# Optimization experiments

Hardware: AMD Instinct MI355X
Metric: run time of the kernel (lower is better)

## Reference

```python
import jax, jax.numpy as jnp
from jax import lax
import numpy as np

B, S, D, COMP = 4, 1024, 512, 4


def setup_inputs() -> dict:
    key = jax.random.key(0)
    x = jax.random.normal(key, (B * S, D), dtype=jnp.float32)
    return {"x": x, "comp_rate": COMP, "seqlen": S}


def _merge_step(x, t, seq):
    # x: [seq, D], compacted so the k = seq - t valid tokens occupy rows 0..k-1.
    xn = jnp.roll(x, -1, axis=0)  # x[i+1] (wrap value never selected among valid pairs)
    # dist only feeds argmax (non-differentiable), mirror torch exactly; stop_gradient
    # keeps the vjp from saving residuals for this dead-for-gradients path.
    xg = lax.stop_gradient(x)
    dist = jnp.sum(xg * jnp.roll(xg, -1, axis=0), axis=-1)  # scalar_product metric
    j = jnp.arange(x.shape[0])
    dist = jnp.where(j < seq - 1 - t, dist, -jnp.inf)  # k-1 valid adjacent pairs
    mid = jnp.argmax(dist)
    jm = j[:, None]
    # rows < mid keep, row mid becomes (x[mid]+x[mid+1])/2, rows > mid shift left by 1
    return jnp.where(jm < mid, x, jnp.where(jm == mid, (x + xn) * 0.5, xn))


def _merge_sample(x, steps, seq):
    def body(carry, t):
        return _merge_step(carry, t, seq), None
    x, _ = lax.scan(body, x, jnp.arange(steps))
    return x


def reference(x, comp_rate, seqlen):
    d = x.shape[-1]
    b = x.shape[0] // seqlen
    n_comp = seqlen // comp_rate
    steps = seqlen - n_comp
    xb = x.reshape(b, seqlen, d)
    merged = jax.vmap(lambda xs: _merge_sample(xs, steps, seqlen))(xb)
    # torch smart_merge concatenates per-sample results along dim 0
    return merged[:, :n_comp].reshape(b * n_comp, d)
```

## Files before the change

kernel.cpp:

```cpp
#include <hip/hip_runtime.h>
#include <math.h>

#define S 1024
#define D 512
#define NCOMP (S / 4)
#define STEPS (S - NCOMP)
#define NEG_INF (-__builtin_inff())

__device__ __forceinline__ int   f2i(float x) { return __builtin_bit_cast(int, x); }
__device__ __forceinline__ float i2f(int x)   { return __builtin_bit_cast(float, x); }

__device__ __forceinline__ unsigned fkey(float f) {
    unsigned u = __builtin_bit_cast(unsigned, f);
    return (u & 0x80000000u) ? ~u : (u | 0x80000000u);
}
__device__ __forceinline__ float unfkey(unsigned k) {
    unsigned u = (k & 0x80000000u) ? (k & 0x7fffffffu) : ~k;
    return __builtin_bit_cast(float, u);
}

__device__ __forceinline__ float wave_sum63(float x) {
    x += i2f(__builtin_amdgcn_update_dpp(0, f2i(x), 0x111, 0xF, 0xF, true));
    x += i2f(__builtin_amdgcn_update_dpp(0, f2i(x), 0x112, 0xF, 0xF, true));
    x += i2f(__builtin_amdgcn_update_dpp(0, f2i(x), 0x114, 0xF, 0xF, true));
    x += i2f(__builtin_amdgcn_update_dpp(0, f2i(x), 0x118, 0xF, 0xF, true));
    x += i2f(__builtin_amdgcn_update_dpp(0, f2i(x), 0x142, 0xA, 0xF, true));
    x += i2f(__builtin_amdgcn_update_dpp(0, f2i(x), 0x143, 0xC, 0xF, true));
    return x;
}

#define AMAX_STEP(ctrl, rm) do {                                                        \
    unsigned ok_ = (unsigned)__builtin_amdgcn_update_dpp((int)key, (int)key, (ctrl), (rm), 0xF, false); \
    int      oi_ = __builtin_amdgcn_update_dpp(bi, bi, (ctrl), (rm), 0xF, false);        \
    bool tk_ = (ok_ > key) || ((ok_ == key) && (oi_ < bi));                              \
    key = tk_ ? ok_ : key; bi = tk_ ? oi_ : bi;                                          \
} while (0)

struct Row { float4 a, b; };

__device__ __forceinline__ Row row_load(const float* vals, int slot, int lane) {
    const float4* p = (const float4*)(vals + (size_t)slot * D);
    Row r; r.a = p[lane * 2]; r.b = p[lane * 2 + 1]; return r;
}
__device__ __forceinline__ void row_store(float* vals, int slot, int lane, Row r) {
    float4* p = (float4*)(vals + (size_t)slot * D);
    p[lane * 2] = r.a; p[lane * 2 + 1] = r.b;
}
__device__ __forceinline__ Row row_avg(Row x, Row y) {
    Row r;
    r.a.x = (x.a.x + y.a.x) * 0.5f; r.a.y = (x.a.y + y.a.y) * 0.5f;
    r.a.z = (x.a.z + y.a.z) * 0.5f; r.a.w = (x.a.w + y.a.w) * 0.5f;
    r.b.x = (x.b.x + y.b.x) * 0.5f; r.b.y = (x.b.y + y.b.y) * 0.5f;
    r.b.z = (x.b.z + y.b.z) * 0.5f; r.b.w = (x.b.w + y.b.w) * 0.5f;
    return r;
}
__device__ __forceinline__ float dot8_partial(Row x, Row y) {
    float acc = x.a.x * y.a.x;
    acc += x.a.y * y.a.y; acc += x.a.z * y.a.z; acc += x.a.w * y.a.w;
    acc += x.b.x * y.b.x; acc += x.b.y * y.b.y; acc += x.b.z * y.b.z; acc += x.b.w * y.b.w;
    return acc;
}
__device__ __forceinline__ int lsr(int s) { return ((unsigned)s < (unsigned)S) ? s : 0; }
__device__ __forceinline__ int lsl(int s) { return ((unsigned)s <= (unsigned)S) ? s : 0; }

__device__ __forceinline__ void lds_argmax(const float* dist, int lane, float& v1, int& i1) {
    float av[16];
#pragma unroll
    for (int k = 0; k < 16; ++k) av[k] = dist[lane + 64 * k];
    float v8[8]; int k8[8];
#pragma unroll
    for (int k = 0; k < 8; ++k) { bool tk = av[k+8] > av[k]; v8[k] = tk ? av[k+8] : av[k]; k8[k] = tk ? (k+8) : k; }
    float v4[4]; int k4[4];
#pragma unroll
    for (int k = 0; k < 4; ++k) { bool tk = v8[k+4] > v8[k]; v4[k] = tk ? v8[k+4] : v8[k]; k4[k] = tk ? k8[k+4] : k8[k]; }
    float v2[2]; int k2[2];
#pragma unroll
    for (int k = 0; k < 2; ++k) { bool tk = v4[k+2] > v4[k]; v2[k] = tk ? v4[k+2] : v4[k]; k2[k] = tk ? k4[k+2] : k4[k]; }
    bool tk1 = v2[1] > v2[0];
    float lv = tk1 ? v2[1] : v2[0];
    int   lk = tk1 ? k2[1] : k2[0];
    unsigned key = fkey(lv);
    int bi = lane | (lk << 6);
    AMAX_STEP(0x111, 0xF); AMAX_STEP(0x112, 0xF);
    AMAX_STEP(0x114, 0xF); AMAX_STEP(0x118, 0xF);
    AMAX_STEP(0x142, 0xA); AMAX_STEP(0x143, 0xC);
    i1 = __builtin_amdgcn_readlane(bi, 63);
    v1 = unfkey((unsigned)__builtin_amdgcn_readlane((int)key, 63));
}

__global__ __launch_bounds__(256) void init_kernel(const float* __restrict__ x,
                                                   float* __restrict__ vals,
                                                   float* __restrict__ out) {
    const int blk = blockIdx.x, b = blk >> 4, g = blk & 15;
    const int tid = threadIdx.x, lane = tid & 63, w = tid >> 6;
    const float* xb = x + (size_t)b * S * D;
    if (vals != x) {
        float* vb = vals + (size_t)b * S * D;
        const float4* s4 = (const float4*)xb;
        float4* d4 = (float4*)vb;
        const int base = g * (S * D / 4 / 16);
        for (int i = tid; i < S * D / 4 / 16; i += 256) d4[base + i] = s4[base + i];
    }
    float* sd = out + (size_t)b * NCOMP * D;
#pragma unroll 1
    for (int j = 0; j < 16; ++j) {
        int pr = g * 64 + w * 16 + j;
        if (pr < S - 1) {
            Row A = row_load(xb, pr, lane);
            Row B = row_load(xb, pr + 1, lane);
            float t = wave_sum63(dot8_partial(A, B));
            if (lane == 63) sd[pr] = t;
        }
    }
    if (g == 0 && tid == 0) sd[S - 1] = NEG_INF;
}

__global__ __launch_bounds__(64) void merge_kernel(float* __restrict__ vals,
                                                   float* __restrict__ out) {
    const int b = blockIdx.x, lane = threadIdx.x;
    float* vb = vals + (size_t)b * S * D;
    float* aux = out + (size_t)b * NCOMP * D;
    const float* sd = aux;
    int* outIdx = (int*)(aux + S);

    __shared__ int4  links[S + 1];
    __shared__ float dist[S];

#pragma unroll
    for (int k = 0; k < 16; ++k) {
        int s = lane + 64 * k;
        links[s] = make_int4(s - 1, s + 1, (s + 2 <= S) ? (s + 2) : S, 0);
        dist[s] = sd[s];
    }
    if (lane == 0) links[S] = make_int4(S, S, S, 0);

    float v1; int i1;
    lds_argmax(dist, lane, v1, i1);
    int m = i1;
    int4 L0 = links[m];
    int p = __builtin_amdgcn_readfirstlane(L0.x);
    int r = __builtin_amdgcn_readfirstlane(L0.y);
    int q = __builtin_amdgcn_readfirstlane(L0.z);
    bool hasp = (p >= 0), hasq = (q < S);
    int pp = hasp ? __builtin_amdgcn_readfirstlane(links[p].x) : -1;
    int nq = hasq ? __builtin_amdgcn_readfirstlane(links[q].y) : S;
    Row Rp  = row_load(vb, lsr(p),  lane);
    Row Rm  = row_load(vb, m,       lane);
    Row Rr  = row_load(vb, r,       lane);
    Row Rq  = row_load(vb, lsr(q),  lane);
    Row Rpp = row_load(vb, lsr(pp), lane);
    Row Rnq = row_load(vb, lsr(nq), lane);

#pragma unroll 1
    for (int t = 0; t < STEPS; ++t) {
        if (lane == 0) {
            links[m].y = q; links[m].z = nq;
            if (hasp) links[p].z = q;
            if (hasq) links[q].x = m;
            dist[m] = NEG_INF; dist[r] = NEG_INF;
            if (hasp) dist[p] = NEG_INF;
        }
        Row vm = row_avg(Rm, Rr);
        row_store(vb, m, lane, vm);
        if (t + 1 >= STEPS) break;

        float sp_ = wave_sum63(dot8_partial(Rp, vm));
        float sq_ = wave_sum63(dot8_partial(vm, Rq));
        float ndp = hasp ? i2f(__builtin_amdgcn_readlane(f2i(sp_), 63)) : NEG_INF;
        float ndm = hasq ? i2f(__builtin_amdgcn_readlane(f2i(sq_), 63)) : NEG_INF;

        lds_argmax(dist, lane, v1, i1);

        float best = v1; int bi = i1;
        if (hasp && (ndp > best || (ndp == best && p < bi))) { best = ndp; bi = p; }
        if (hasq && (ndm > best || (ndm == best && m < bi))) { best = ndm; bi = m; }
        const int m2 = bi;

        if (lane == 0) {
            if (hasp) dist[p] = ndp;
            if (hasq) dist[m] = ndm;
        }

        int4 Li = links[lsl(i1)];
        int p2 = __builtin_amdgcn_readfirstlane(Li.x);
        int r2 = __builtin_amdgcn_readfirstlane(Li.y);
        int q2 = __builtin_amdgcn_readfirstlane(Li.z);
        int4 Lp2 = links[lsl(p2)];
        int4 Lq2 = links[lsl(q2)];
        int pp2 = (p2 >= 0) ? __builtin_amdgcn_readfirstlane(Lp2.x) : -1;
        int nq2 = (q2 < S)  ? __builtin_amdgcn_readfirstlane(Lq2.y) : S;
        Row Sp  = (p2 == m)  ? vm : row_load(vb, lsr(p2),  lane);
        Row Si  = row_load(vb, lsr(i1), lane);
        Row Sr  = row_load(vb, lsr(r2), lane);
        Row Sq  = (q2 == m)  ? vm : row_load(vb, lsr(q2),  lane);
        Row Spp = (pp2 == m) ? vm : row_load(vb, lsr(pp2), lane);
        Row Snq = (nq2 == m) ? vm : row_load(vb, lsr(nq2), lane);

        if (m2 == m) {
            int nnq = S;
            if (nq < S) nnq = __builtin_amdgcn_readfirstlane(links[nq].y);
            Row Rnq2 = (nnq < S) ? row_load(vb, lsr(nnq), lane) : Rnq;
            Rm = vm; Rr = Rq; Rq = Rnq; Rnq = Rnq2;
            r = q; q = nq; nq = nnq;
            hasq = (q < S);
        } else if (m2 == p) {
            int npp = -1;
            if (pp >= 0) npp = __builtin_amdgcn_readfirstlane(links[pp].x);
            Row Rpp2 = (npp >= 0) ? row_load(vb, lsr(npp), lane) : Rpp;
            Rr = vm; Rm = Rp; Rp = Rpp; Rpp = Rpp2;
            r = m; m = p; p = pp; pp = npp;
            hasp = (p >= 0);
        } else {
            m = i1; p = p2; r = r2; q = q2; pp = pp2; nq = nq2;
            Rm = Si; Rr = Sr; Rp = Sp; Rq = Sq; Rpp = Spp; Rnq = Snq;
            hasp = (p >= 0); hasq = (q < S);
        }
    }

    if (lane == 0) {
        int s = 0;
        for (int i = 0; i < NCOMP; i += 2) {
            outIdx[i] = s;
            int4 Ls = links[s];
            if (i + 1 < NCOMP) outIdx[i + 1] = Ls.y;
            s = Ls.z;
        }
    }
}

__global__ __launch_bounds__(256) void gather_kernel(const float* __restrict__ vals,
                                                     float* __restrict__ out) {
    const int b = blockIdx.x, part = blockIdx.y;
    const float* vb = vals + (size_t)b * S * D;
    float* ob = out + (size_t)b * NCOMP * D;
    __shared__ int oi[NCOMP / 8];
    const int row0 = part * (NCOMP / 8);
    if (threadIdx.x < NCOMP / 8)
        oi[threadIdx.x] = ((const int*)(ob + S))[row0 + threadIdx.x];
    __syncthreads();
    const float4* v4 = (const float4*)vb;
    float4* o4 = (float4*)ob;
    const int per = (NCOMP / 8) * (D / 4);
    for (int idx = threadIdx.x; idx < per; idx += 256) {
        int row = idx >> 7, c = idx & 127;
        o4[(size_t)(row0 + row) * (D / 4) + c] = v4[(size_t)oi[row] * (D / 4) + c];
    }
}

extern "C" void kernel_launch(void* const* d_in, const int* in_sizes, int n_in,
                              void* d_out, int out_size, void* d_ws, size_t ws_size,
                              hipStream_t stream) {
    const float* x = (const float*)d_in[0];
    float* out = (float*)d_out;
    const int b = in_sizes[0] / (S * D);
    const size_t need = (size_t)in_sizes[0] * sizeof(float);
    float* vals = (ws_size >= need) ? (float*)d_ws : (float*)x;
    init_kernel<<<dim3(16 * b), dim3(256), 0, stream>>>(x, vals, out);
    merge_kernel<<<dim3(b), dim3(64), 0, stream>>>(vals, out);
    gather_kernel<<<dim3(b, 8), dim3(256), 0, stream>>>(vals, out);
}
```

Measured before the change: 1.052 ms.

## Fuse init, merge and gather into one kernel with wave-specialized merge loop

Replaces the three kernels with a single 512-thread block per sample. The copy, the initial distance computation and the final gather move inside it, and the serial merge loop is split between two waves: one does the row averaging and neighbour dot products, the other does the incremental argmax and link updates. A per-lane cached column max limits LDS rescans to lanes whose column was invalidated. This removes the launch overhead and the six speculative row loads per step, at the cost of two block-wide barriers per step and only 4 blocks on the whole GPU for the init and gather phases.

```diff
diff --git a/kernel.cpp b/kernel.cpp
--- a/kernel.cpp
+++ b/kernel.cpp
@@ -9,6 +9,7 @@
 
 __device__ __forceinline__ int   f2i(float x) { return __builtin_bit_cast(int, x); }
 __device__ __forceinline__ float i2f(int x)   { return __builtin_bit_cast(float, x); }
+__device__ __forceinline__ int   rfl(int x)   { return __builtin_amdgcn_readfirstlane(x); }
 
 __device__ __forceinline__ unsigned fkey(float f) {
     unsigned u = __builtin_bit_cast(unsigned, f);
@@ -63,10 +64,7 @@
 __device__ __forceinline__ int lsr(int s) { return ((unsigned)s < (unsigned)S) ? s : 0; }
 __device__ __forceinline__ int lsl(int s) { return ((unsigned)s <= (unsigned)S) ? s : 0; }
 
-__device__ __forceinline__ void lds_argmax(const float* dist, int lane, float& v1, int& i1) {
-    float av[16];
-#pragma unroll
-    for (int k = 0; k < 16; ++k) av[k] = dist[lane + 64 * k];
+__device__ __forceinline__ void tree16(const float (&av)[16], float& cm, int& ca) {
     float v8[8]; int k8[8];
 #pragma unroll
     for (int k = 0; k < 8; ++k) { bool tk = av[k+8] > av[k]; v8[k] = tk ? av[k+8] : av[k]; k8[k] = tk ? (k+8) : k; }
@@ -77,173 +75,168 @@
 #pragma unroll
     for (int k = 0; k < 2; ++k) { bool tk = v4[k+2] > v4[k]; v2[k] = tk ? v4[k+2] : v4[k]; k2[k] = tk ? k4[k+2] : k4[k]; }
     bool tk1 = v2[1] > v2[0];
-    float lv = tk1 ? v2[1] : v2[0];
-    int   lk = tk1 ? k2[1] : k2[0];
-    unsigned key = fkey(lv);
-    int bi = lane | (lk << 6);
-    AMAX_STEP(0x111, 0xF); AMAX_STEP(0x112, 0xF);
-    AMAX_STEP(0x114, 0xF); AMAX_STEP(0x118, 0xF);
-    AMAX_STEP(0x142, 0xA); AMAX_STEP(0x143, 0xC);
-    i1 = __builtin_amdgcn_readlane(bi, 63);
-    v1 = unfkey((unsigned)__builtin_amdgcn_readlane((int)key, 63));
-}
-
-__global__ __launch_bounds__(256) void init_kernel(const float* __restrict__ x,
-                                                   float* __restrict__ vals,
-                                                   float* __restrict__ out) {
-    const int blk = blockIdx.x, b = blk >> 4, g = blk & 15;
-    const int tid = threadIdx.x, lane = tid & 63, w = tid >> 6;
+    cm = tk1 ? v2[1] : v2[0];
+    ca = tk1 ? k2[1] : k2[0];
+}
+
+__global__ __launch_bounds__(512, 1) void pool_kernel(const float* __restrict__ x,
+                                                      float* __restrict__ out,
+                                                      float* vals_base) {
+    const int b = blockIdx.x, tid = threadIdx.x, lane = tid & 63, wave = tid >> 6;
+    float* vb = vals_base + (size_t)b * S * D;
     const float* xb = x + (size_t)b * S * D;
-    if (vals != x) {
-        float* vb = vals + (size_t)b * S * D;
+
+    __shared__ int4  links[S + 1];
+    __shared__ float dist[S];
+    __shared__ float mbA[2];
+    __shared__ int   mbB[4];
+    __shared__ int   outIdx[NCOMP];
+
+    if (vals_base != x) {
         const float4* s4 = (const float4*)xb;
         float4* d4 = (float4*)vb;
-        const int base = g * (S * D / 4 / 16);
-        for (int i = tid; i < S * D / 4 / 16; i += 256) d4[base + i] = s4[base + i];
-    }
-    float* sd = out + (size_t)b * NCOMP * D;
-#pragma unroll 1
-    for (int j = 0; j < 16; ++j) {
-        int pr = g * 64 + w * 16 + j;
-        if (pr < S - 1) {
-            Row A = row_load(xb, pr, lane);
-            Row B = row_load(xb, pr + 1, lane);
-            float t = wave_sum63(dot8_partial(A, B));
-            if (lane == 63) sd[pr] = t;
-        }
-    }
-    if (g == 0 && tid == 0) sd[S - 1] = NEG_INF;
-}
-
-__global__ __launch_bounds__(64) void merge_kernel(float* __restrict__ vals,
-                                                   float* __restrict__ out) {
-    const int b = blockIdx.x, lane = threadIdx.x;
-    float* vb = vals + (size_t)b * S * D;
-    float* aux = out + (size_t)b * NCOMP * D;
-    const float* sd = aux;
-    int* outIdx = (int*)(aux + S);
-
-    __shared__ int4  links[S + 1];
-    __shared__ float dist[S];
-
-#pragma unroll
-    for (int k = 0; k < 16; ++k) {
-        int s = lane + 64 * k;
-        links[s] = make_int4(s - 1, s + 1, (s + 2 <= S) ? (s + 2) : S, 0);
-        dist[s] = sd[s];
-    }
-    if (lane == 0) links[S] = make_int4(S, S, S, 0);
-
-    float v1; int i1;
-    lds_argmax(dist, lane, v1, i1);
-    int m = i1;
-    int4 L0 = links[m];
-    int p = __builtin_amdgcn_readfirstlane(L0.x);
-    int r = __builtin_amdgcn_readfirstlane(L0.y);
-    int q = __builtin_amdgcn_readfirstlane(L0.z);
-    bool hasp = (p >= 0), hasq = (q < S);
-    int pp = hasp ? __builtin_amdgcn_readfirstlane(links[p].x) : -1;
-    int nq = hasq ? __builtin_amdgcn_readfirstlane(links[q].y) : S;
-    Row Rp  = row_load(vb, lsr(p),  lane);
-    Row Rm  = row_load(vb, m,       lane);
-    Row Rr  = row_load(vb, r,       lane);
-    Row Rq  = row_load(vb, lsr(q),  lane);
-    Row Rpp = row_load(vb, lsr(pp), lane);
-    Row Rnq = row_load(vb, lsr(nq), lane);
-
+        for (int i = tid; i < S * D / 4; i += 512) d4[i] = s4[i];
+    }
+    for (int s = tid; s <= S; s += 512)
+        links[s] = (s == S) ? make_int4(S, S, S, 0)
+                            : make_int4(s - 1, s + 1, (s + 2 <= S) ? (s + 2) : S, 0);
+    __syncthreads();
+
+    for (int pr = wave; pr < S - 1; pr += 8) {
+        Row A = row_load(vb, pr, lane);
+        Row B = row_load(vb, pr + 1, lane);
+        float t_ = wave_sum63(dot8_partial(A, B));
+        if (lane == 63) dist[pr] = t_;
+    }
+    if (tid == 0) dist[S - 1] = NEG_INF;
+    __syncthreads();
+
+    float cm = NEG_INF; int ca = 0;
+    int m = 0, p = -1, r = 0, q = S, pp = -1, nq = S;
+    bool hasp = false, hasq = false;
+    if (wave == 0) {
+        float av[16];
+#pragma unroll
+        for (int k = 0; k < 16; ++k) av[k] = dist[lane + 64 * k];
+        tree16(av, cm, ca);
+        unsigned key = fkey(cm); int bi = lane | (ca << 6);
+        AMAX_STEP(0x111, 0xF); AMAX_STEP(0x112, 0xF);
+        AMAX_STEP(0x114, 0xF); AMAX_STEP(0x118, 0xF);
+        AMAX_STEP(0x142, 0xA); AMAX_STEP(0x143, 0xC);
+        m = __builtin_amdgcn_readlane(bi, 63);
+        int4 Lm = links[m];
+        p = rfl(Lm.x); r = rfl(Lm.y); q = rfl(Lm.z);
+        hasp = (p >= 0); hasq = (q < S);
+        pp = hasp ? rfl(links[lsl(p)].x) : -1;
+        nq = rfl(links[r].z);
+        if (lane == 0) { mbB[0] = m; mbB[1] = p; mbB[2] = r; mbB[3] = q; }
+    }
+    __syncthreads();
+
+    int pm = -7, ppv = -7, pqv = -7;
+    Row vmP, RpP, RqP;
 #pragma unroll 1
     for (int t = 0; t < STEPS; ++t) {
-        if (lane == 0) {
-            links[m].y = q; links[m].z = nq;
-            if (hasp) links[p].z = q;
-            if (hasq) links[q].x = m;
-            dist[m] = NEG_INF; dist[r] = NEG_INF;
-            if (hasp) dist[p] = NEG_INF;
+        int i1v = 0, pi = -1, ri = 0, qi = S;
+        float v1 = NEG_INF;
+        if (wave == 1) {
+            int m1 = rfl(mbB[0]), p1 = rfl(mbB[1]), r1 = rfl(mbB[2]), q1 = rfl(mbB[3]);
+            bool h_p = (p1 >= 0), h_q = (q1 < S);
+            Row Rm, Rr, Rp, Rq;
+            if (m1 == pm) {
+                Rm = vmP; Rr = RqP; Rp = RpP;
+                Rq = row_load(vb, lsr(q1), lane);
+            } else if (r1 == pm) {
+                Rm = RpP; Rr = vmP; Rq = RqP;
+                Rp = row_load(vb, lsr(p1), lane);
+            } else {
+                Rm = row_load(vb, m1, lane);
+                Rr = row_load(vb, r1, lane);
+                Rp = (p1 == pm) ? vmP : row_load(vb, lsr(p1), lane);
+                Rq = (q1 == pm) ? vmP : row_load(vb, lsr(q1), lane);
+            }
+            Row vm = row_avg(Rm, Rr);
+            row_store(vb, m1, lane, vm);
+            float sp = wave_sum63(dot8_partial(Rp, vm));
+            float sq = wave_sum63(dot8_partial(vm, Rq));
+            if (lane == 63) { mbA[0] = h_p ? sp : NEG_INF; mbA[1] = h_q ? sq : NEG_INF; }
+            pm = m1; ppv = p1; pqv = q1; vmP = vm; RpP = Rp; RqP = Rq;
+            (void)ppv; (void)pqv;
+        } else if (wave == 0) {
+            if (lane == 0) {
+                if (hasp) dist[p] = NEG_INF;
+                dist[m] = NEG_INF; dist[r] = NEG_INF;
+            }
+            bool needR = (lane == (m & 63) && ca == (m >> 6)) ||
+                         (lane == (r & 63) && ca == (r >> 6)) ||
+                         (hasp && lane == (p & 63) && ca == (p >> 6));
+            if (needR) {
+                float av[16];
+#pragma unroll
+                for (int k = 0; k < 16; ++k) av[k] = dist[lane + 64 * k];
+                tree16(av, cm, ca);
+            }
+            if (lane == 0) {
+                links[m].y = q; links[m].z = nq;
+                if (hasp) links[p].z = q;
+                if (hasq) links[q].x = m;
+            }
+            unsigned key = fkey(cm); int bi = lane | (ca << 6);
+            AMAX_STEP(0x111, 0xF); AMAX_STEP(0x112, 0xF);
+            AMAX_STEP(0x114, 0xF); AMAX_STEP(0x118, 0xF);
+            AMAX_STEP(0x142, 0xA); AMAX_STEP(0x143, 0xC);
+            i1v = __builtin_amdgcn_readlane(bi, 63);
+            v1  = unfkey((unsigned)__builtin_amdgcn_readlane((int)key, 63));
+            int4 Li = links[i1v];
+            pi = rfl(Li.x); ri = rfl(Li.y); qi = rfl(Li.z);
         }
-        Row vm = row_avg(Rm, Rr);
-        row_store(vb, m, lane, vm);
-        if (t + 1 >= STEPS) break;
-
-        float sp_ = wave_sum63(dot8_partial(Rp, vm));
-        float sq_ = wave_sum63(dot8_partial(vm, Rq));
-        float ndp = hasp ? i2f(__builtin_amdgcn_readlane(f2i(sp_), 63)) : NEG_INF;
-        float ndm = hasq ? i2f(__builtin_amdgcn_readlane(f2i(sq_), 63)) : NEG_INF;
-
-        lds_argmax(dist, lane, v1, i1);
-
-        float best = v1; int bi = i1;
-        if (hasp && (ndp > best || (ndp == best && p < bi))) { best = ndp; bi = p; }
-        if (hasq && (ndm > best || (ndm == best && m < bi))) { best = ndm; bi = m; }
-        const int m2 = bi;
-
-        if (lane == 0) {
-            if (hasp) dist[p] = ndp;
-            if (hasq) dist[m] = ndm;
-        }
-
-        int4 Li = links[lsl(i1)];
-        int p2 = __builtin_amdgcn_readfirstlane(Li.x);
-        int r2 = __builtin_amdgcn_readfirstlane(Li.y);
-        int q2 = __builtin_amdgcn_readfirstlane(Li.z);
-        int4 Lp2 = links[lsl(p2)];
-        int4 Lq2 = links[lsl(q2)];
-        int pp2 = (p2 >= 0) ? __builtin_amdgcn_readfirstlane(Lp2.x) : -1;
-        int nq2 = (q2 < S)  ? __builtin_amdgcn_readfirstlane(Lq2.y) : S;
-        Row Sp  = (p2 == m)  ? vm : row_load(vb, lsr(p2),  lane);
-        Row Si  = row_load(vb, lsr(i1), lane);
-        Row Sr  = row_load(vb, lsr(r2), lane);
-        Row Sq  = (q2 == m)  ? vm : row_load(vb, lsr(q2),  lane);
-        Row Spp = (pp2 == m) ? vm : row_load(vb, lsr(pp2), lane);
-        Row Snq = (nq2 == m) ? vm : row_load(vb, lsr(nq2), lane);
-
-        if (m2 == m) {
-            int nnq = S;
-            if (nq < S) nnq = __builtin_amdgcn_readfirstlane(links[nq].y);
-            Row Rnq2 = (nnq < S) ? row_load(vb, lsr(nnq), lane) : Rnq;
-            Rm = vm; Rr = Rq; Rq = Rnq; Rnq = Rnq2;
-            r = q; q = nq; nq = nnq;
-            hasq = (q < S);
-        } else if (m2 == p) {
-            int npp = -1;
-            if (pp >= 0) npp = __builtin_amdgcn_readfirstlane(links[pp].x);
-            Row Rpp2 = (npp >= 0) ? row_load(vb, lsr(npp), lane) : Rpp;
-            Rr = vm; Rm = Rp; Rp = Rpp; Rpp = Rpp2;
-            r = m; m = p; p = pp; pp = npp;
-            hasp = (p >= 0);
-        } else {
-            m = i1; p = p2; r = r2; q = q2; pp = pp2; nq = nq2;
-            Rm = Si; Rr = Sr; Rp = Sp; Rq = Sq; Rpp = Spp; Rnq = Snq;
+        __syncthreads();
+        if (wave == 0) {
+            float ndp = mbA[0], ndm = mbA[1];
+            if (lane == 0) {
+                if (hasp) dist[p] = ndp;
+                if (hasq) dist[m] = ndm;
+            }
+            if (hasp && lane == (p & 63)) {
+                int kp = p >> 6;
+                if (ndp > cm || (ndp == cm && kp < ca)) { cm = ndp; ca = kp; }
+            }
+            if (hasq && lane == (m & 63)) {
+                int km = m >> 6;
+                if (ndm > cm || (ndm == cm && km < ca)) { cm = ndm; ca = km; }
+            }
+            float best = v1; int b2 = i1v;
+            if (hasp && (ndp > best || (ndp == best && p < b2))) { best = ndp; b2 = p; }
+            if (hasq && (ndm > best || (ndm == best && m < b2))) { best = ndm; b2 = m; }
+            int m2 = rfl(b2);
+            int p2, r2, q2;
+            if (m2 == m)      { p2 = p;  r2 = q; q2 = nq; }
+            else if (m2 == p) { p2 = pp; r2 = m; q2 = q;  }
+            else              { p2 = pi; r2 = ri; q2 = qi; }
+            int pp2 = (p2 >= 0) ? rfl(links[lsl(p2)].x) : -1;
+            int nq2 = rfl(links[r2].z);
+            if (lane == 0) { mbB[0] = m2; mbB[1] = p2; mbB[2] = r2; mbB[3] = q2; }
+            m = m2; p = p2; r = r2; q = q2; pp = pp2; nq = nq2;
             hasp = (p >= 0); hasq = (q < S);
         }
-    }
-
-    if (lane == 0) {
+        __syncthreads();
+    }
+
+    if (wave == 0 && lane == 0) {
         int s = 0;
         for (int i = 0; i < NCOMP; i += 2) {
+            int4 Ls = links[s];
             outIdx[i] = s;
-            int4 Ls = links[s];
             if (i + 1 < NCOMP) outIdx[i + 1] = Ls.y;
             s = Ls.z;
         }
     }
-}
-
-__global__ __launch_bounds__(256) void gather_kernel(const float* __restrict__ vals,
-                                                     float* __restrict__ out) {
-    const int b = blockIdx.x, part = blockIdx.y;
-    const float* vb = vals + (size_t)b * S * D;
+    __syncthreads();
+
     float* ob = out + (size_t)b * NCOMP * D;
-    __shared__ int oi[NCOMP / 8];
-    const int row0 = part * (NCOMP / 8);
-    if (threadIdx.x < NCOMP / 8)
-        oi[threadIdx.x] = ((const int*)(ob + S))[row0 + threadIdx.x];
-    __syncthreads();
-    const float4* v4 = (const float4*)vb;
-    float4* o4 = (float4*)ob;
-    const int per = (NCOMP / 8) * (D / 4);
-    for (int idx = threadIdx.x; idx < per; idx += 256) {
-        int row = idx >> 7, c = idx & 127;
-        o4[(size_t)(row0 + row) * (D / 4) + c] = v4[(size_t)oi[row] * (D / 4) + c];
+    for (int i = wave; i < NCOMP; i += 8) {
+        Row rr = row_load(vb, outIdx[i], lane);
+        row_store(ob, i, lane, rr);
     }
 }
 
@@ -255,7 +248,5 @@
     const int b = in_sizes[0] / (S * D);
     const size_t need = (size_t)in_sizes[0] * sizeof(float);
     float* vals = (ws_size >= need) ? (float*)d_ws : (float*)x;
-    init_kernel<<<dim3(16 * b), dim3(256), 0, stream>>>(x, vals, out);
-    merge_kernel<<<dim3(b), dim3(64), 0, stream>>>(vals, out);
-    gather_kernel<<<dim3(b, 8), dim3(256), 0, stream>>>(vals, out);
-}
+    pool_kernel<<<dim3(b), dim3(512), 0, stream>>>(x, out, vals);
+}
```

Result: slower. 1.345 ms (+27.9%).

## Keep pair distances in registers with contiguous slot ownership and drop speculative row loads

Applied to the files above, without the earlier changes.

Pair distances now live in per-lane registers as order-preserving unsigned keys. Each lane owns 16 contiguous slots, so the LDS dist array and its per-step reloads are gone, and single-slot updates go through a lane-predicated switch. The argmax becomes a register tree, then a wave max, then a ballot that picks the lowest tied lane, instead of a dual-value DPP argmax. The speculative prefetch of six candidate rows, with its three-way branch, is replaced by loading the four needed rows after the argmax, reusing the last averaged row when it is a neighbour. This shortens the serial per-step path but puts global row loads back onto the critical path each step.

```diff
diff --git a/kernel.cpp b/kernel.cpp
--- a/kernel.cpp
+++ b/kernel.cpp
@@ -9,14 +9,11 @@
 
 __device__ __forceinline__ int   f2i(float x) { return __builtin_bit_cast(int, x); }
 __device__ __forceinline__ float i2f(int x)   { return __builtin_bit_cast(float, x); }
+__device__ __forceinline__ int   rfl(int x)   { return __builtin_amdgcn_readfirstlane(x); }
 
 __device__ __forceinline__ unsigned fkey(float f) {
     unsigned u = __builtin_bit_cast(unsigned, f);
     return (u & 0x80000000u) ? ~u : (u | 0x80000000u);
-}
-__device__ __forceinline__ float unfkey(unsigned k) {
-    unsigned u = (k & 0x80000000u) ? (k & 0x7fffffffu) : ~k;
-    return __builtin_bit_cast(float, u);
 }
 
 __device__ __forceinline__ float wave_sum63(float x) {
@@ -29,12 +26,13 @@
     return x;
 }
 
-#define AMAX_STEP(ctrl, rm) do {                                                        \
-    unsigned ok_ = (unsigned)__builtin_amdgcn_update_dpp((int)key, (int)key, (ctrl), (rm), 0xF, false); \
-    int      oi_ = __builtin_amdgcn_update_dpp(bi, bi, (ctrl), (rm), 0xF, false);        \
-    bool tk_ = (ok_ > key) || ((ok_ == key) && (oi_ < bi));                              \
-    key = tk_ ? ok_ : key; bi = tk_ ? oi_ : bi;                                          \
-} while (0)
+__device__ __forceinline__ unsigned wave_max63(unsigned x) {
+#define MAXD(c, rm) { unsigned o_ = (unsigned)__builtin_amdgcn_update_dpp(0, (int)x, (c), (rm), 0xF, true); x = (x > o_) ? x : o_; }
+    MAXD(0x111, 0xF) MAXD(0x112, 0xF) MAXD(0x114, 0xF)
+    MAXD(0x118, 0xF) MAXD(0x142, 0xA) MAXD(0x143, 0xC)
+#undef MAXD
+    return x;
+}
 
 struct Row { float4 a, b; };
 
@@ -63,29 +61,34 @@
 __device__ __forceinline__ int lsr(int s) { return ((unsigned)s < (unsigned)S) ? s : 0; }
 __device__ __forceinline__ int lsl(int s) { return ((unsigned)s <= (unsigned)S) ? s : 0; }
 
-__device__ __forceinline__ void lds_argmax(const float* dist, int lane, float& v1, int& i1) {
-    float av[16];
-#pragma unroll
-    for (int k = 0; k < 16; ++k) av[k] = dist[lane + 64 * k];
-    float v8[8]; int k8[8];
+__device__ __forceinline__ void tree16k(const unsigned (&av)[16], unsigned& cm, int& ca) {
+    unsigned v8[8]; int k8[8];
 #pragma unroll
     for (int k = 0; k < 8; ++k) { bool tk = av[k+8] > av[k]; v8[k] = tk ? av[k+8] : av[k]; k8[k] = tk ? (k+8) : k; }
-    float v4[4]; int k4[4];
+    unsigned v4[4]; int k4[4];
 #pragma unroll
     for (int k = 0; k < 4; ++k) { bool tk = v8[k+4] > v8[k]; v4[k] = tk ? v8[k+4] : v8[k]; k4[k] = tk ? k8[k+4] : k8[k]; }
-    float v2[2]; int k2[2];
+    unsigned v2[2]; int k2[2];
 #pragma unroll
     for (int k = 0; k < 2; ++k) { bool tk = v4[k+2] > v4[k]; v2[k] = tk ? v4[k+2] : v4[k]; k2[k] = tk ? k4[k+2] : k4[k]; }
     bool tk1 = v2[1] > v2[0];
-    float lv = tk1 ? v2[1] : v2[0];
-    int   lk = tk1 ? k2[1] : k2[0];
-    unsigned key = fkey(lv);
-    int bi = lane | (lk << 6);
-    AMAX_STEP(0x111, 0xF); AMAX_STEP(0x112, 0xF);
-    AMAX_STEP(0x114, 0xF); AMAX_STEP(0x118, 0xF);
-    AMAX_STEP(0x142, 0xA); AMAX_STEP(0x143, 0xC);
-    i1 = __builtin_amdgcn_readlane(bi, 63);
-    v1 = unfkey((unsigned)__builtin_amdgcn_readlane((int)key, 63));
+    cm = tk1 ? v2[1] : v2[0];
+    ca = tk1 ? k2[1] : k2[0];
+}
+
+__device__ __forceinline__ void upd(unsigned (&av)[16], int lane, int slot, unsigned key) {
+    if (lane == (slot >> 4)) {
+        switch (slot & 15) {
+            case 0:  av[0]  = key; break;  case 1:  av[1]  = key; break;
+            case 2:  av[2]  = key; break;  case 3:  av[3]  = key; break;
+            case 4:  av[4]  = key; break;  case 5:  av[5]  = key; break;
+            case 6:  av[6]  = key; break;  case 7:  av[7]  = key; break;
+            case 8:  av[8]  = key; break;  case 9:  av[9]  = key; break;
+            case 10: av[10] = key; break;  case 11: av[11] = key; break;
+            case 12: av[12] = key; break;  case 13: av[13] = key; break;
+            case 14: av[14] = key; break;  case 15: av[15] = key; break;
+        }
+    }
 }
 
 __global__ __launch_bounds__(256) void init_kernel(const float* __restrict__ x,
@@ -115,113 +118,95 @@
     if (g == 0 && tid == 0) sd[S - 1] = NEG_INF;
 }
 
-__global__ __launch_bounds__(64) void merge_kernel(float* __restrict__ vals,
-                                                   float* __restrict__ out) {
+__global__ __launch_bounds__(64, 1) void merge_kernel(float* __restrict__ vals,
+                                                      float* __restrict__ out) {
     const int b = blockIdx.x, lane = threadIdx.x;
     float* vb = vals + (size_t)b * S * D;
     float* aux = out + (size_t)b * NCOMP * D;
-    const float* sd = aux;
     int* outIdx = (int*)(aux + S);
 
-    __shared__ int4  links[S + 1];
-    __shared__ float dist[S];
-
-#pragma unroll
-    for (int k = 0; k < 16; ++k) {
-        int s = lane + 64 * k;
-        links[s] = make_int4(s - 1, s + 1, (s + 2 <= S) ? (s + 2) : S, 0);
-        dist[s] = sd[s];
-    }
-    if (lane == 0) links[S] = make_int4(S, S, S, 0);
-
-    float v1; int i1;
-    lds_argmax(dist, lane, v1, i1);
-    int m = i1;
-    int4 L0 = links[m];
-    int p = __builtin_amdgcn_readfirstlane(L0.x);
-    int r = __builtin_amdgcn_readfirstlane(L0.y);
-    int q = __builtin_amdgcn_readfirstlane(L0.z);
-    bool hasp = (p >= 0), hasq = (q < S);
-    int pp = hasp ? __builtin_amdgcn_readfirstlane(links[p].x) : -1;
-    int nq = hasq ? __builtin_amdgcn_readfirstlane(links[q].y) : S;
-    Row Rp  = row_load(vb, lsr(p),  lane);
-    Row Rm  = row_load(vb, m,       lane);
-    Row Rr  = row_load(vb, r,       lane);
-    Row Rq  = row_load(vb, lsr(q),  lane);
-    Row Rpp = row_load(vb, lsr(pp), lane);
-    Row Rnq = row_load(vb, lsr(nq), lane);
+    __shared__ int4 links[S + 1];
+    for (int s = lane; s <= S; s += 64)
+        links[s] = (s >= S) ? make_int4(S, S, S, 0)
+                            : make_int4(s - 1, s + 1, (s + 2 <= S) ? (s + 2) : S, 0);
+
+    unsigned av[16];
+    {
+        const float4* sd4 = (const float4*)aux;
+#pragma unroll
+        for (int j = 0; j < 4; ++j) {
+            float4 v = sd4[lane * 4 + j];
+            av[4*j+0] = fkey(v.x); av[4*j+1] = fkey(v.y);
+            av[4*j+2] = fkey(v.z); av[4*j+3] = fkey(v.w);
+        }
+    }
+
+    unsigned cm; int ca;
+    tree16k(av, cm, ca);
+    unsigned smax = (unsigned)__builtin_amdgcn_readlane((int)wave_max63(cm), 63);
+    unsigned long long tied = __ballot(cm == smax);
+    int wl = (int)__ffsll(tied) - 1;
+    int m = rfl((wl << 4) | __builtin_amdgcn_readlane(ca, wl));
+    int4 Lm = links[m];
+    int p = rfl(Lm.x), r = rfl(Lm.y), q = rfl(Lm.z);
+    int nq = rfl(links[lsl(q)].y);
+    Row Rp = row_load(vb, lsr(p), lane);
+    Row Rm = row_load(vb, m,      lane);
+    Row Rr = row_load(vb, r,      lane);
+    Row Rq = row_load(vb, lsr(q), lane);
+    int mprev = -1;
+    Row vmPrev = Rm;
 
 #pragma unroll 1
-    for (int t = 0; t < STEPS; ++t) {
+    for (int t = 0; ; ++t) {
+        const bool hasp = (p >= 0), hasq = (q < S);
+        if (p == mprev) Rp = vmPrev;
+        if (m == mprev) Rm = vmPrev;
+        if (r == mprev) Rr = vmPrev;
+        if (q == mprev) Rq = vmPrev;
+
+        Row vm = row_avg(Rm, Rr);
+        row_store(vb, m, lane, vm);
+
+        float sp = wave_sum63(dot8_partial(Rp, vm));
+        float sq = wave_sum63(dot8_partial(vm, Rq));
+        unsigned ndpk = hasp ? fkey(i2f(__builtin_amdgcn_readlane(f2i(sp), 63))) : 0u;
+        unsigned ndmk = hasq ? fkey(i2f(__builtin_amdgcn_readlane(f2i(sq), 63))) : 0u;
+
         if (lane == 0) {
             links[m].y = q; links[m].z = nq;
             if (hasp) links[p].z = q;
             if (hasq) links[q].x = m;
-            dist[m] = NEG_INF; dist[r] = NEG_INF;
-            if (hasp) dist[p] = NEG_INF;
-        }
-        Row vm = row_avg(Rm, Rr);
-        row_store(vb, m, lane, vm);
-        if (t + 1 >= STEPS) break;
-
-        float sp_ = wave_sum63(dot8_partial(Rp, vm));
-        float sq_ = wave_sum63(dot8_partial(vm, Rq));
-        float ndp = hasp ? i2f(__builtin_amdgcn_readlane(f2i(sp_), 63)) : NEG_INF;
-        float ndm = hasq ? i2f(__builtin_amdgcn_readlane(f2i(sq_), 63)) : NEG_INF;
-
-        lds_argmax(dist, lane, v1, i1);
-
-        float best = v1; int bi = i1;
-        if (hasp && (ndp > best || (ndp == best && p < bi))) { best = ndp; bi = p; }
-        if (hasq && (ndm > best || (ndm == best && m < bi))) { best = ndm; bi = m; }
-        const int m2 = bi;
-
-        if (lane == 0) {
-            if (hasp) dist[p] = ndp;
-            if (hasq) dist[m] = ndm;
-        }
-
-        int4 Li = links[lsl(i1)];
-        int p2 = __builtin_amdgcn_readfirstlane(Li.x);
-        int r2 = __builtin_amdgcn_readfirstlane(Li.y);
-        int q2 = __builtin_amdgcn_readfirstlane(Li.z);
-        int4 Lp2 = links[lsl(p2)];
-        int4 Lq2 = links[lsl(q2)];
-        int pp2 = (p2 >= 0) ? __builtin_amdgcn_readfirstlane(Lp2.x) : -1;
-        int nq2 = (q2 < S)  ? __builtin_amdgcn_readfirstlane(Lq2.y) : S;
-        Row Sp  = (p2 == m)  ? vm : row_load(vb, lsr(p2),  lane);
-        Row Si  = row_load(vb, lsr(i1), lane);
-        Row Sr  = row_load(vb, lsr(r2), lane);
-        Row Sq  = (q2 == m)  ? vm : row_load(vb, lsr(q2),  lane);
-        Row Spp = (pp2 == m) ? vm : row_load(vb, lsr(pp2), lane);
-        Row Snq = (nq2 == m) ? vm : row_load(vb, lsr(nq2), lane);
-
-        if (m2 == m) {
-            int nnq = S;
-            if (nq < S) nnq = __builtin_amdgcn_readfirstlane(links[nq].y);
-            Row Rnq2 = (nnq < S) ? row_load(vb, lsr(nnq), lane) : Rnq;
-            Rm = vm; Rr = Rq; Rq = Rnq; Rnq = Rnq2;
-            r = q; q = nq; nq = nnq;
-            hasq = (q < S);
-        } else if (m2 == p) {
-            int npp = -1;
-            if (pp >= 0) npp = __builtin_amdgcn_readfirstlane(links[pp].x);
-            Row Rpp2 = (npp >= 0) ? row_load(vb, lsr(npp), lane) : Rpp;
-            Rr = vm; Rm = Rp; Rp = Rpp; Rpp = Rpp2;
-            r = m; m = p; p = pp; pp = npp;
-            hasp = (p >= 0);
-        } else {
-            m = i1; p = p2; r = r2; q = q2; pp = pp2; nq = nq2;
-            Rm = Si; Rr = Sr; Rp = Sp; Rq = Sq; Rpp = Spp; Rnq = Snq;
-            hasp = (p >= 0); hasq = (q < S);
-        }
+        }
+        upd(av, lane, r, 0u);
+        upd(av, lane, m, ndmk);
+        if (hasp) upd(av, lane, p, ndpk);
+
+        if (t == STEPS - 1) break;
+
+        tree16k(av, cm, ca);
+        smax = (unsigned)__builtin_amdgcn_readlane((int)wave_max63(cm), 63);
+        tied = __ballot(cm == smax);
+        wl = (int)__ffsll(tied) - 1;
+        int m2 = rfl((wl << 4) | __builtin_amdgcn_readlane(ca, wl));
+
+        int4 L2 = links[m2];
+        int p2 = rfl(L2.x), r2 = rfl(L2.y), q2 = rfl(L2.z);
+        int nq2 = rfl(links[lsl(q2)].y);
+        Rp = row_load(vb, lsr(p2), lane);
+        Rm = row_load(vb, m2,      lane);
+        Rr = row_load(vb, r2,      lane);
+        Rq = row_load(vb, lsr(q2), lane);
+
+        mprev = m; vmPrev = vm;
+        m = m2; p = p2; r = r2; q = q2; nq = nq2;
     }
 
     if (lane == 0) {
         int s = 0;
         for (int i = 0; i < NCOMP; i += 2) {
+            int4 Ls = links[s];
             outIdx[i] = s;
-            int4 Ls = links[s];
             if (i + 1 < NCOMP) outIdx[i + 1] = Ls.y;
             s = Ls.z;
         }
```

After: 1.092 ms. 1.04x slower.
